# Optimization experiments

Hardware: AMD Instinct MI355X
Metric: run time of the kernel (lower is better)

Reference implementation:

```python
import jax, jax.numpy as jnp
import numpy as np

B, N, C, H = 2, 256, 512, 8
D = C // H
SCALER = 1.0 / np.sqrt(D)


def setup_inputs() -> dict:
    key = jax.random.key(0)
    k1, k2 = jax.random.split(key)
    hidden_state = jax.random.normal(k1, (B, N, C), dtype=jnp.float32)
    # Linear(C -> 5C), no bias. Torch Linear stores W as [out, in]; y = x @ W.T
    W = jax.random.normal(k2, (5 * C, C), dtype=jnp.float32) * np.float32(1.0 / np.sqrt(C))
    return {"hidden_state": hidden_state, "W": W}


def reference(hidden_state, W):
    b_, n, c = hidden_state.shape
    w = hidden_state @ W.T                                   # [B,N,5C]
    w = w.reshape(b_, n, 5, H, D).transpose(2, 0, 3, 1, 4)   # [5,B,H,N,D]
    a, bq, cq, v1, v2 = w[0], w[1], w[2], w[3], w[4]

    # Pairwise score matrices with the (unscaled) clamped position bias min(j-i,0).
    # NOTE: the original code computes ALiBi slopes / position_bias_encoder but never
    # adds them to X/Y/Z -- only `position_bias` is added. We replicate that exactly.
    idx = jnp.arange(n)
    pb = jnp.minimum(idx[None, :] - idx[:, None], 0).astype(hidden_state.dtype)  # [N,N]

    X = jnp.einsum('bhid,bhjd->bhij', a, bq) * SCALER + pb   # [B,H,N,N]
    Y = jnp.einsum('bhjd,bhkd->bhjk', bq, cq) * SCALER + pb
    Z = jnp.einsum('bhkd,bhid->bhki', cq, a) * SCALER + pb

    # 3-way stabilized exponentials (axis choices match the torch code)
    X = jnp.exp(X - jnp.max(X, axis=-1, keepdims=True))
    Y = jnp.exp(Y - jnp.max(Y, axis=(-2, -1), keepdims=True))
    Z = jnp.exp(Z - jnp.max(Z, axis=-2, keepdims=True))

    # up_{id} = sum_{j,k} X_ij Y_jk Z_ki v1_jd v2_kd  (V = outer(v1, v2) is implicit)
    T = jnp.einsum('bhij,bhjk,bhjd->bhikd', X, Y, v1)        # [B,H,N,N,D]
    up = jnp.einsum('bhikd,bhki,bhkd->bhid', T, Z, v2)       # [B,H,N,D]

    down = jnp.einsum('bhij,bhjk,bhki->bhi', X, Y, Z) + 1e-9 # [B,H,N]
    att = up / down[..., None]
    return att.transpose(0, 2, 1, 3).reshape(b_, n, c)       # [B,N,C]
```

## Files before the change

kernel.cpp:

```cpp
#include <hip/hip_runtime.h>
#include <math.h>

#define NN 256
#define HH 8
#define DD 64
#define BH 16
#define SCALER 0.125f

#define REG     (BH*NN*DD)
#define MAT_SZ  (BH*NN*NN)
#define OFF_XH  0
#define OFF_V1T 524288
#define OFF_QKV 0
#define OFF_X   1310720
#define OFF_Y   (OFF_X + MAT_SZ)
#define OFF_Z   (OFF_Y + MAT_SZ)
#define OFF_MX  (OFF_Z + MAT_SZ)
#define OFF_MY  (OFF_MX + BH*NN)
#define OFF_MZ  (OFF_MY + 16)
#define OFF_YT  4464656
#define OFF_V2T 4988944
#define KB      4
#define OFF_UP  5251088
#define OFF_DN  6299664
#define OFF_YR  6316048

typedef _Float16 f16x8 __attribute__((ext_vector_type(8)));
typedef _Float16 f16x4 __attribute__((ext_vector_type(4)));
typedef float    f32x4 __attribute__((ext_vector_type(4)));

__global__ __launch_bounds__(256) void k_proj(const float* __restrict__ Hs,
                                              const float* __restrict__ W,
                                              float* __restrict__ qkv) {
  __shared__ float As[16][68];
  __shared__ float Bs[16][68];
  const int bx = blockIdx.x, by = blockIdx.y;
  const int tid = threadIdx.x;
  const int ri = tid >> 4, ci = tid & 15;
  const int o0 = bx * 64, m0 = by * 64;
  float acc[4][4] = {};
  for (int k0 = 0; k0 < 512; k0 += 16) {
    __syncthreads();
    {
      const int m = tid >> 2, kq = (tid & 3) * 4;
      float4 va = *(const float4*)&Hs[(m0 + m) * 512 + k0 + kq];
      As[kq + 0][m] = va.x; As[kq + 1][m] = va.y; As[kq + 2][m] = va.z; As[kq + 3][m] = va.w;
      float4 vb = *(const float4*)&W[(o0 + m) * 512 + k0 + kq];
      Bs[kq + 0][m] = vb.x; Bs[kq + 1][m] = vb.y; Bs[kq + 2][m] = vb.z; Bs[kq + 3][m] = vb.w;
    }
    __syncthreads();
#pragma unroll
    for (int kk = 0; kk < 16; ++kk) {
      float4 a = *(const float4*)&As[kk][ri * 4];
      float4 b = *(const float4*)&Bs[kk][ci * 4];
      acc[0][0] += a.x * b.x; acc[0][1] += a.x * b.y; acc[0][2] += a.x * b.z; acc[0][3] += a.x * b.w;
      acc[1][0] += a.y * b.x; acc[1][1] += a.y * b.y; acc[1][2] += a.y * b.z; acc[1][3] += a.y * b.w;
      acc[2][0] += a.z * b.x; acc[2][1] += a.z * b.y; acc[2][2] += a.z * b.z; acc[2][3] += a.z * b.w;
      acc[3][0] += a.w * b.x; acc[3][1] += a.w * b.y; acc[3][2] += a.w * b.z; acc[3][3] += a.w * b.w;
    }
  }
  const int p = o0 >> 9;
  const int h = (o0 >> 6) & 7;
  const int d0 = ci * 4;
#pragma unroll
  for (int l = 0; l < 4; ++l) {
    const int r = m0 + ri * 4 + l;
    const int b = r >> 8, n = r & 255;
    float* dst = qkv + p * REG + (b * 8 + h) * (NN * DD) + n * DD + d0;
    *(float4*)dst = make_float4(acc[l][0], acc[l][1], acc[l][2], acc[l][3]);
  }
}

__global__ __launch_bounds__(256) void k_scores(const float* __restrict__ qkv,
                                                float* __restrict__ ws) {
  __shared__ float Us[32][68];
  __shared__ float Ws_[32][68];
  const int ms = blockIdx.z, bh = blockIdx.y;
  const int tr = blockIdx.x >> 3, tc = blockIdx.x & 7;
  const float* U; const float* Wm; float* O;
  if (ms == 0)      { U = qkv + 0 * REG; Wm = qkv + 1 * REG; O = ws + OFF_X; }
  else if (ms == 1) { U = qkv + 1 * REG; Wm = qkv + 2 * REG; O = ws + OFF_Y; }
  else              { U = qkv + 2 * REG; Wm = qkv + 0 * REG; O = ws + OFF_Z; }
  U  += bh * (NN * DD);
  Wm += bh * (NN * DD);
  O  += bh * (NN * NN);
  const int i0 = tr * 32, k0 = tc * 32;
  const int tid = threadIdx.x;
  {
    const int r = tid >> 3, d8 = (tid & 7) * 8;
    *(float4*)&Us[r][d8]      = *(const float4*)&U[(i0 + r) * DD + d8];
    *(float4*)&Us[r][d8 + 4]  = *(const float4*)&U[(i0 + r) * DD + d8 + 4];
    *(float4*)&Ws_[r][d8]     = *(const float4*)&Wm[(k0 + r) * DD + d8];
    *(float4*)&Ws_[r][d8 + 4] = *(const float4*)&Wm[(k0 + r) * DD + d8 + 4];
  }
  __syncthreads();
  const int ri = tid >> 4, ci = tid & 15;
  float a00 = 0.f, a01 = 0.f, a10 = 0.f, a11 = 0.f;
#pragma unroll
  for (int dd = 0; dd < 16; ++dd) {
    float4 u0 = *(const float4*)&Us[ri][dd * 4];
    float4 u1 = *(const float4*)&Us[ri + 16][dd * 4];
    float4 w0 = *(const float4*)&Ws_[ci][dd * 4];
    float4 w1 = *(const float4*)&Ws_[ci + 16][dd * 4];
    a00 += u0.x * w0.x + u0.y * w0.y + u0.z * w0.z + u0.w * w0.w;
    a01 += u0.x * w1.x + u0.y * w1.y + u0.z * w1.z + u0.w * w1.w;
    a10 += u1.x * w0.x + u1.y * w0.y + u1.z * w0.z + u1.w * w0.w;
    a11 += u1.x * w1.x + u1.y * w1.y + u1.z * w1.z + u1.w * w1.w;
  }
#define STORE_SC(accv, rr, cc) { \
    int row = (rr), col = (cc); \
    O[row * NN + col] = (accv) * SCALER + fminf((float)(col - row), 0.f); }
  STORE_SC(a00, i0 + ri,      k0 + ci)
  STORE_SC(a01, i0 + ri,      k0 + ci + 16)
  STORE_SC(a10, i0 + ri + 16, k0 + ci)
  STORE_SC(a11, i0 + ri + 16, k0 + ci + 16)
#undef STORE_SC
}

__global__ __launch_bounds__(256) void k_maxes(const float* __restrict__ ws,
                                               float* __restrict__ mx,
                                               float* __restrict__ yrow,
                                               float* __restrict__ mz) {
  const int blk = blockIdx.x, tid = threadIdx.x;
  if (blk < 2048) {
    const int wid = tid >> 6, lane = tid & 63;
    const float* base = ws + (blk < 1024 ? OFF_X : OFF_Y);
    float* out = (blk < 1024) ? mx : yrow;
    const int gr = (blk & 1023) * 4 + wid;
    float4 v = *(const float4*)&base[gr * 256 + lane * 4];
    float m = fmaxf(fmaxf(v.x, v.y), fmaxf(v.z, v.w));
#pragma unroll
    for (int off = 32; off; off >>= 1) m = fmaxf(m, __shfl_xor(m, off));
    if (lane == 0) out[gr] = m;
  } else {
    const int b2 = blk - 2048;
    const int bh = b2 >> 2, ic = b2 & 3;
    const int il = tid & 63, kp = tid >> 6;
    const int i = ic * 64 + il;
    const float* Zb = ws + OFF_Z;
    float m = -3.4e38f;
    for (int k = kp; k < 256; k += 4) m = fmaxf(m, Zb[bh * (NN * NN) + k * NN + i]);
    __shared__ float red[4][64];
    red[kp][il] = m;
    __syncthreads();
    if (kp == 0)
      mz[bh * NN + i] = fmaxf(fmaxf(red[0][il], red[1][il]), fmaxf(red[2][il], red[3][il]));
  }
}

__global__ __launch_bounds__(256) void k_ymax2(const float* __restrict__ yrow, float* __restrict__ my) {
  const int bh = blockIdx.x, tid = threadIdx.x;
  float m = yrow[bh * 256 + tid];
#pragma unroll
  for (int off = 32; off; off >>= 1) m = fmaxf(m, __shfl_xor(m, off));
  __shared__ float red[4];
  if ((tid & 63) == 0) red[tid >> 6] = m;
  __syncthreads();
  if (tid == 0) my[bh] = fmaxf(fmaxf(red[0], red[1]), fmaxf(red[2], red[3]));
}

__global__ __launch_bounds__(256) void k_cvtexp(float* __restrict__ ws) {
  __shared__ float T[64][65];
  const int blk = blockIdx.x, tid = threadIdx.x;
  if (blk < 256) {
    const float* X = ws + OFF_X;
    _Float16* Xh = (_Float16*)(ws + OFF_XH);
    const int gt = blk * 256 + tid;
    const int base = gt * 16;
    const float s = ws[OFF_MX + (gt >> 4)];
#pragma unroll
    for (int q = 0; q < 4; ++q) {
      float4 v = *(const float4*)&X[base + q * 4];
      f16x4 o = {(_Float16)expf(v.x - s), (_Float16)expf(v.y - s),
                 (_Float16)expf(v.z - s), (_Float16)expf(v.w - s)};
      *(f16x4*)&Xh[base + q * 4] = o;
    }
  } else if (blk < 512) {
    const int b2 = blk - 256;
    const int bh = b2 >> 4, jt = (b2 >> 2) & 3, kt = b2 & 3;
    const float* Y = ws + OFF_Y + bh * 65536;
    _Float16* Yt = (_Float16*)(ws + OFF_YT) + bh * 65536;
    const float s = ws[OFF_MY + bh];
    const int j0 = jt * 64, k0 = kt * 64;
#pragma unroll 4
    for (int p = 0; p < 16; ++p) {
      const int idx = p * 256 + tid, r = idx >> 6, c = idx & 63;
      T[r][c] = Y[(j0 + r) * 256 + k0 + c];
    }
    __syncthreads();
#pragma unroll 4
    for (int p = 0; p < 16; ++p) {
      const int idx = p * 256 + tid, r = idx >> 6, c = idx & 63;
      Yt[(k0 + r) * 256 + j0 + c] = (_Float16)expf(T[c][r] - s);
    }
  } else if (blk < 576) {
    const int b2 = blk - 512;
    const int bh = b2 >> 2, jt = b2 & 3;
    const float* v1 = ws + OFF_QKV + 3 * REG + bh * 16384;
    _Float16* v1t = (_Float16*)(ws + OFF_V1T) + bh * 16384;
    const int j0 = jt * 64;
#pragma unroll 4
    for (int p = 0; p < 16; ++p) {
      const int idx = p * 256 + tid, r = idx >> 6, c = idx & 63;
      T[r][c] = v1[(j0 + r) * 64 + c];
    }
    __syncthreads();
#pragma unroll 4
    for (int p = 0; p < 16; ++p) {
      const int idx = p * 256 + tid, r = idx >> 6, c = idx & 63;
      v1t[r * 256 + j0 + c] = (_Float16)T[c][r];
    }
  } else if (blk < 640) {
    const int b2 = blk - 576;
    const int bh = b2 >> 2, kt = b2 & 3;
    const float* v2 = ws + OFF_QKV + 4 * REG + bh * 16384;
    float* v2t = ws + OFF_V2T + bh * 16384;
    const int k0 = kt * 64;
#pragma unroll 4
    for (int p = 0; p < 16; ++p) {
      const int idx = p * 256 + tid, r = idx >> 6, c = idx & 63;
      T[r][c] = v2[(k0 + r) * 64 + c];
    }
    __syncthreads();
#pragma unroll 4
    for (int p = 0; p < 16; ++p) {
      const int idx = p * 256 + tid, r = idx >> 6, c = idx & 63;
      v2t[r * 256 + k0 + c] = T[c][r];
    }
  } else {
    const int rem = (blk - 640) * 256 + tid;
    const int bh = rem >> 14, rr = rem & 16383;
    const int c4 = (rr & 63) * 4;
    float4* base = (float4*)(ws + OFF_Z);
    float4 v = base[rem];
    float4 s = *(const float4*)&ws[OFF_MZ + bh * NN + c4];
    v.x = expf(v.x - s.x); v.y = expf(v.y - s.y); v.z = expf(v.z - s.z); v.w = expf(v.w - s.w);
    base[rem] = v;
  }
}

__global__ __launch_bounds__(512) void k_heavy(const float* __restrict__ ws,
                                               float* __restrict__ upP,
                                               float* __restrict__ dnP) {
  const int kb = blockIdx.x, ib = blockIdx.y, zz = blockIdx.z;
  const int bh = zz >> 2, dp = zz & 3;
  const int k0 = kb * 64, i0 = ib * 64, d0 = dp * 16;
  const int tid = threadIdx.x;
  const int w = tid >> 6, lane = tid & 63;
  const int k16 = w & 3, ihalf = w >> 2;
  const int li = lane & 15, grp = lane >> 4;

  __shared__ _Float16 v1s[16 * 256];
  __shared__ float v2s[16 * 64];
  __shared__ float up_l[4][64][20];
  __shared__ float dn_l[4][64];

  const _Float16* Xh  = (const _Float16*)(ws + OFF_XH);
  const _Float16* Yt  = (const _Float16*)(ws + OFF_YT);
  const _Float16* v1t = (const _Float16*)(ws + OFF_V1T);
  const float*    v2t = ws + OFF_V2T;
  const float*    Zp  = ws + OFF_Z + bh * 65536;

  {
    const float4* src = (const float4*)(v1t + bh * 16384 + d0 * 256);
    ((float4*)v1s)[tid] = src[tid];
  }
  if (tid < 256) {
    const int d = tid >> 4, kq = (tid & 15) * 4;
    *(float4*)&v2s[d * 64 + kq] = *(const float4*)&v2t[bh * 16384 + (d0 + d) * 256 + k0 + kq];
  }

  f16x8 Yf[8];
  {
    const _Float16* yb = Yt + (long)bh * 65536 + (k0 + k16 * 16 + li) * 256 + grp * 8;
#pragma unroll
    for (int js = 0; js < 8; ++js) Yf[js] = *(const f16x8*)(yb + js * 32);
  }
  f16x8 Xf0[8], Xf1[8];
  {
    const _Float16* xb0 = Xh + (long)bh * 65536 + (i0 + (ihalf * 2 + 0) * 16 + li) * 256 + grp * 8;
    const _Float16* xb1 = Xh + (long)bh * 65536 + (i0 + (ihalf * 2 + 1) * 16 + li) * 256 + grp * 8;
#pragma unroll
    for (int js = 0; js < 8; ++js) { Xf0[js] = *(const f16x8*)(xb0 + js * 32); Xf1[js] = *(const f16x8*)(xb1 + js * 32); }
  }
  float Zr0[4], Zr1[4];
#pragma unroll
  for (int r = 0; r < 4; ++r) {
    const int kk = (k0 + k16 * 16 + grp * 4 + r) * 256 + i0;
    Zr0[r] = Zp[kk + (ihalf * 2 + 0) * 16 + li];
    Zr1[r] = Zp[kk + (ihalf * 2 + 1) * 16 + li];
  }

  __syncthreads();

  const int ir0 = (ihalf * 2 + 0) * 16 + li;
  const int ir1 = (ihalf * 2 + 1) * 16 + li;

  for (int it = 0; it < 16; ++it) {
    f32x4 acc0 = {0.f, 0.f, 0.f, 0.f}, acc1 = {0.f, 0.f, 0.f, 0.f};
#pragma unroll
    for (int js = 0; js < 8; ++js) {
      f16x8 vf = *(const f16x8*)&v1s[it * 256 + js * 32 + grp * 8];
      f16x8 ad = Yf[js] * vf;
      acc0 = __builtin_amdgcn_mfma_f32_16x16x32_f16(ad, Xf0[js], acc0, 0, 0, 0);
      acc1 = __builtin_amdgcn_mfma_f32_16x16x32_f16(ad, Xf1[js], acc1, 0, 0, 0);
    }
    f32x4 w2 = *(const f32x4*)&v2s[it * 64 + k16 * 16 + grp * 4];
    float s0 = (acc0[0] * Zr0[0]) * w2[0] + (acc0[1] * Zr0[1]) * w2[1]
             + (acc0[2] * Zr0[2]) * w2[2] + (acc0[3] * Zr0[3]) * w2[3];
    float s1 = (acc1[0] * Zr1[0]) * w2[0] + (acc1[1] * Zr1[1]) * w2[1]
             + (acc1[2] * Zr1[2]) * w2[2] + (acc1[3] * Zr1[3]) * w2[3];
    s0 += __shfl_xor(s0, 16); s0 += __shfl_xor(s0, 32);
    s1 += __shfl_xor(s1, 16); s1 += __shfl_xor(s1, 32);
    if (lane < 16) {
      up_l[k16][ir0][it] = s0;
      up_l[k16][ir1][it] = s1;
    }
  }
  if (dp == 3) {
    f32x4 acc0 = {0.f, 0.f, 0.f, 0.f}, acc1 = {0.f, 0.f, 0.f, 0.f};
#pragma unroll
    for (int js = 0; js < 8; ++js) {
      acc0 = __builtin_amdgcn_mfma_f32_16x16x32_f16(Yf[js], Xf0[js], acc0, 0, 0, 0);
      acc1 = __builtin_amdgcn_mfma_f32_16x16x32_f16(Yf[js], Xf1[js], acc1, 0, 0, 0);
    }
    float s0 = acc0[0] * Zr0[0] + acc0[1] * Zr0[1] + acc0[2] * Zr0[2] + acc0[3] * Zr0[3];
    float s1 = acc1[0] * Zr1[0] + acc1[1] * Zr1[1] + acc1[2] * Zr1[2] + acc1[3] * Zr1[3];
    s0 += __shfl_xor(s0, 16); s0 += __shfl_xor(s0, 32);
    s1 += __shfl_xor(s1, 16); s1 += __shfl_xor(s1, 32);
    if (lane < 16) {
      dn_l[k16][ir0] = s0;
      dn_l[k16][ir1] = s1;
    }
  }
  __syncthreads();
  {
    const int il = tid >> 3, dq = (tid & 7) * 2;
    float a = up_l[0][il][dq]     + up_l[1][il][dq]     + up_l[2][il][dq]     + up_l[3][il][dq];
    float b = up_l[0][il][dq + 1] + up_l[1][il][dq + 1] + up_l[2][il][dq + 1] + up_l[3][il][dq + 1];
    float* dst = upP + ((long)((kb * 16 + bh) * 256) + i0 + il) * 64 + d0 + dq;
    dst[0] = a; dst[1] = b;
  }
  if (dp == 3 && tid < 64)
    dnP[(kb * 16 + bh) * 256 + i0 + tid] =
        dn_l[0][tid] + dn_l[1][tid] + dn_l[2][tid] + dn_l[3][tid];
}

__global__ __launch_bounds__(256) void k_final(const float* __restrict__ ws_in, float* __restrict__ out) {
  const int g = blockIdx.x * 256 + threadIdx.x;
  const int e0 = g * 4;
  const int c = e0 & 511, n = (e0 >> 9) & 255, b = e0 >> 17;
  const int h = c >> 6, d = c & 63;
  const int bh = b * 8 + h;
  const float* upP = ws_in + OFF_UP;
  const float* dnP = ws_in + OFF_DN;
  float4 acc = make_float4(0.f, 0.f, 0.f, 0.f);
  float dn = 0.f;
#pragma unroll
  for (int ks = 0; ks < KB; ++ks) {
    const float4 u = *(const float4*)&upP[((ks * 16 + bh) * 256 + n) * 64 + d];
    acc.x += u.x; acc.y += u.y; acc.z += u.z; acc.w += u.w;
    dn += dnP[(ks * 16 + bh) * 256 + n];
  }
  const float inv = 1.f / (dn + 1e-9f);
  acc.x *= inv; acc.y *= inv; acc.z *= inv; acc.w *= inv;
  *(float4*)&out[e0] = acc;
}

extern "C" void kernel_launch(void* const* d_in, const int* in_sizes, int n_in,
                              void* d_out, int out_size, void* d_ws, size_t ws_size,
                              hipStream_t stream) {
  (void)in_sizes; (void)n_in; (void)out_size; (void)ws_size;
  const float* hidden = (const float*)d_in[0];
  const float* W      = (const float*)d_in[1];
  float* ws  = (float*)d_ws;
  float* out = (float*)d_out;

  k_proj<<<dim3(40, 8), 256, 0, stream>>>(hidden, W, ws + OFF_QKV);
  k_scores<<<dim3(64, BH, 3), 256, 0, stream>>>(ws + OFF_QKV, ws);
  k_maxes<<<dim3(2112), 256, 0, stream>>>(ws, ws + OFF_MX, ws + OFF_YR, ws + OFF_MZ);
  k_ymax2<<<dim3(16), 256, 0, stream>>>(ws + OFF_YR, ws + OFF_MY);
  k_cvtexp<<<dim3(1664), 256, 0, stream>>>(ws);
  k_heavy<<<dim3(KB, 4, 64), 512, 0, stream>>>(ws, ws + OFF_UP, ws + OFF_DN);
  k_final<<<dim3(256), 256, 0, stream>>>(ws, out);
}
```

Baseline: 191.4 us.

## Split heavy kernel waves over d instead of i rows, reuse Y*v1 across four X tiles

Each wave now handles all four 16-row i tiles and half of the 16 d columns, instead of two i tiles and all d columns. The Y*v1 elementwise product and the v1 LDS load are reused across four MFMAs rather than two, which halves the loop trip count per wave and gives more independent MFMA chains. The denominator path is restricted to one wave group. Holding X fragments for four tiles raises register pressure, and launch_bounds(512,2) is added to try to keep two blocks resident per CU, which may force spills.

```diff
diff --git a/kernel.cpp b/kernel.cpp
--- a/kernel.cpp
+++ b/kernel.cpp
@@ -239,15 +239,15 @@
   }
 }
 
-__global__ __launch_bounds__(512) void k_heavy(const float* __restrict__ ws,
-                                               float* __restrict__ upP,
-                                               float* __restrict__ dnP) {
+__global__ __launch_bounds__(512, 2) void k_heavy(const float* __restrict__ ws,
+                                                  float* __restrict__ upP,
+                                                  float* __restrict__ dnP) {
   const int kb = blockIdx.x, ib = blockIdx.y, zz = blockIdx.z;
   const int bh = zz >> 2, dp = zz & 3;
   const int k0 = kb * 64, i0 = ib * 64, d0 = dp * 16;
   const int tid = threadIdx.x;
   const int w = tid >> 6, lane = tid & 63;
-  const int k16 = w & 3, ihalf = w >> 2;
+  const int k16 = w & 3, dsub = w >> 2;
   const int li = lane & 15, grp = lane >> 4;
 
   __shared__ _Float16 v1s[16 * 256];
@@ -276,62 +276,61 @@
 #pragma unroll
     for (int js = 0; js < 8; ++js) Yf[js] = *(const f16x8*)(yb + js * 32);
   }
-  f16x8 Xf0[8], Xf1[8];
-  {
-    const _Float16* xb0 = Xh + (long)bh * 65536 + (i0 + (ihalf * 2 + 0) * 16 + li) * 256 + grp * 8;
-    const _Float16* xb1 = Xh + (long)bh * 65536 + (i0 + (ihalf * 2 + 1) * 16 + li) * 256 + grp * 8;
-#pragma unroll
-    for (int js = 0; js < 8; ++js) { Xf0[js] = *(const f16x8*)(xb0 + js * 32); Xf1[js] = *(const f16x8*)(xb1 + js * 32); }
-  }
-  float Zr0[4], Zr1[4];
-#pragma unroll
-  for (int r = 0; r < 4; ++r) {
-    const int kk = (k0 + k16 * 16 + grp * 4 + r) * 256 + i0;
-    Zr0[r] = Zp[kk + (ihalf * 2 + 0) * 16 + li];
-    Zr1[r] = Zp[kk + (ihalf * 2 + 1) * 16 + li];
-  }
+  f16x8 Xf[4][8];
+#pragma unroll
+  for (int iq = 0; iq < 4; ++iq) {
+    const _Float16* xb = Xh + (long)bh * 65536 + (i0 + iq * 16 + li) * 256 + grp * 8;
+#pragma unroll
+    for (int js = 0; js < 8; ++js) Xf[iq][js] = *(const f16x8*)(xb + js * 32);
+  }
+  float Zr[4][4];
+#pragma unroll
+  for (int iq = 0; iq < 4; ++iq)
+#pragma unroll
+    for (int r = 0; r < 4; ++r)
+      Zr[iq][r] = Zp[(k0 + k16 * 16 + grp * 4 + r) * 256 + i0 + iq * 16 + li];
 
   __syncthreads();
 
-  const int ir0 = (ihalf * 2 + 0) * 16 + li;
-  const int ir1 = (ihalf * 2 + 1) * 16 + li;
-
-  for (int it = 0; it < 16; ++it) {
-    f32x4 acc0 = {0.f, 0.f, 0.f, 0.f}, acc1 = {0.f, 0.f, 0.f, 0.f};
+  for (int dd = 0; dd < 8; ++dd) {
+    const int dloc = dsub * 8 + dd;
+    f32x4 acc0 = {0.f,0.f,0.f,0.f}, acc1 = {0.f,0.f,0.f,0.f};
+    f32x4 acc2 = {0.f,0.f,0.f,0.f}, acc3 = {0.f,0.f,0.f,0.f};
 #pragma unroll
     for (int js = 0; js < 8; ++js) {
-      f16x8 vf = *(const f16x8*)&v1s[it * 256 + js * 32 + grp * 8];
+      f16x8 vf = *(const f16x8*)&v1s[dloc * 256 + js * 32 + grp * 8];
       f16x8 ad = Yf[js] * vf;
-      acc0 = __builtin_amdgcn_mfma_f32_16x16x32_f16(ad, Xf0[js], acc0, 0, 0, 0);
-      acc1 = __builtin_amdgcn_mfma_f32_16x16x32_f16(ad, Xf1[js], acc1, 0, 0, 0);
-    }
-    f32x4 w2 = *(const f32x4*)&v2s[it * 64 + k16 * 16 + grp * 4];
-    float s0 = (acc0[0] * Zr0[0]) * w2[0] + (acc0[1] * Zr0[1]) * w2[1]
-             + (acc0[2] * Zr0[2]) * w2[2] + (acc0[3] * Zr0[3]) * w2[3];
-    float s1 = (acc1[0] * Zr1[0]) * w2[0] + (acc1[1] * Zr1[1]) * w2[1]
-             + (acc1[2] * Zr1[2]) * w2[2] + (acc1[3] * Zr1[3]) * w2[3];
-    s0 += __shfl_xor(s0, 16); s0 += __shfl_xor(s0, 32);
-    s1 += __shfl_xor(s1, 16); s1 += __shfl_xor(s1, 32);
-    if (lane < 16) {
-      up_l[k16][ir0][it] = s0;
-      up_l[k16][ir1][it] = s1;
-    }
-  }
-  if (dp == 3) {
-    f32x4 acc0 = {0.f, 0.f, 0.f, 0.f}, acc1 = {0.f, 0.f, 0.f, 0.f};
+      acc0 = __builtin_amdgcn_mfma_f32_16x16x32_f16(ad, Xf[0][js], acc0, 0, 0, 0);
+      acc1 = __builtin_amdgcn_mfma_f32_16x16x32_f16(ad, Xf[1][js], acc1, 0, 0, 0);
+      acc2 = __builtin_amdgcn_mfma_f32_16x16x32_f16(ad, Xf[2][js], acc2, 0, 0, 0);
+      acc3 = __builtin_amdgcn_mfma_f32_16x16x32_f16(ad, Xf[3][js], acc3, 0, 0, 0);
+    }
+    f32x4 w2 = *(const f32x4*)&v2s[dloc * 64 + k16 * 16 + grp * 4];
+#define EPI(accv, iq) { \
+      float s = (accv[0] * Zr[iq][0]) * w2[0] + (accv[1] * Zr[iq][1]) * w2[1] \
+              + (accv[2] * Zr[iq][2]) * w2[2] + (accv[3] * Zr[iq][3]) * w2[3]; \
+      s += __shfl_xor(s, 16); s += __shfl_xor(s, 32); \
+      if (lane < 16) up_l[k16][iq * 16 + li][dloc] = s; }
+    EPI(acc0, 0) EPI(acc1, 1) EPI(acc2, 2) EPI(acc3, 3)
+#undef EPI
+  }
+  if (dp == 3 && dsub == 1) {
+    f32x4 acc0 = {0.f,0.f,0.f,0.f}, acc1 = {0.f,0.f,0.f,0.f};
+    f32x4 acc2 = {0.f,0.f,0.f,0.f}, acc3 = {0.f,0.f,0.f,0.f};
 #pragma unroll
     for (int js = 0; js < 8; ++js) {
-      acc0 = __builtin_amdgcn_mfma_f32_16x16x32_f16(Yf[js], Xf0[js], acc0, 0, 0, 0);
-      acc1 = __builtin_amdgcn_mfma_f32_16x16x32_f16(Yf[js], Xf1[js], acc1, 0, 0, 0);
-    }
-    float s0 = acc0[0] * Zr0[0] + acc0[1] * Zr0[1] + acc0[2] * Zr0[2] + acc0[3] * Zr0[3];
-    float s1 = acc1[0] * Zr1[0] + acc1[1] * Zr1[1] + acc1[2] * Zr1[2] + acc1[3] * Zr1[3];
-    s0 += __shfl_xor(s0, 16); s0 += __shfl_xor(s0, 32);
-    s1 += __shfl_xor(s1, 16); s1 += __shfl_xor(s1, 32);
-    if (lane < 16) {
-      dn_l[k16][ir0] = s0;
-      dn_l[k16][ir1] = s1;
-    }
+      acc0 = __builtin_amdgcn_mfma_f32_16x16x32_f16(Yf[js], Xf[0][js], acc0, 0, 0, 0);
+      acc1 = __builtin_amdgcn_mfma_f32_16x16x32_f16(Yf[js], Xf[1][js], acc1, 0, 0, 0);
+      acc2 = __builtin_amdgcn_mfma_f32_16x16x32_f16(Yf[js], Xf[2][js], acc2, 0, 0, 0);
+      acc3 = __builtin_amdgcn_mfma_f32_16x16x32_f16(Yf[js], Xf[3][js], acc3, 0, 0, 0);
+    }
+#define EPID(accv, iq) { \
+      float s = accv[0] * Zr[iq][0] + accv[1] * Zr[iq][1] \
+              + accv[2] * Zr[iq][2] + accv[3] * Zr[iq][3]; \
+      s += __shfl_xor(s, 16); s += __shfl_xor(s, 32); \
+      if (lane < 16) dn_l[k16][iq * 16 + li] = s; }
+    EPID(acc0, 0) EPID(acc1, 1) EPID(acc2, 2) EPID(acc3, 3)
+#undef EPID
   }
   __syncthreads();
   {
```

New measurement: 196.2 us. 2.5% more time.
